# Performance work log

Measured on AMD Instinct MI355X. Metric: run time of the kernel, lower is better.

Reference implementation:

```python
import jax, jax.numpy as jnp
import numpy as np

NUM_HEADS = 4
NUM_GROUPS = 32
EPS = 1e-6


def group_norm(x, gamma, beta):
    # x: [b, c, h, w]
    b, c, h, w = x.shape
    xg = x.reshape(b, NUM_GROUPS, c // NUM_GROUPS, h, w)
    mu = xg.mean(axis=(2, 3, 4), keepdims=True)
    var = xg.var(axis=(2, 3, 4), keepdims=True)
    xn = ((xg - mu) * jax.lax.rsqrt(var + EPS)).reshape(b, c, h, w)
    return xn * gamma[None, :, None, None] + beta[None, :, None, None]


def conv1x1(x, W, b):
    # 1x1 conv == per-pixel channel matmul. W: [out_c, in_c], b: [out_c]
    return jnp.einsum('bchw,oc->bohw', x, W) + b[None, :, None, None]


def setup_inputs() -> dict:
    key = jax.random.key(0)
    ks = jax.random.split(key, 8)
    c = 256
    b, h, w = 1, 64, 64
    s = 1.0 / np.sqrt(c)
    return {
        'x_kv': jax.random.normal(ks[0], (b, c, h, w), dtype=jnp.float32),
        'gn_gamma': jnp.ones((c,), dtype=jnp.float32),
        'gn_beta': jnp.zeros((c,), dtype=jnp.float32),
        'Wq': jax.random.normal(ks[1], (c, c), dtype=jnp.float32) * s,
        'bq': jnp.zeros((c,), dtype=jnp.float32),
        'Wk': jax.random.normal(ks[2], (c, c), dtype=jnp.float32) * s,
        'bk': jnp.zeros((c,), dtype=jnp.float32),
        'Wv': jax.random.normal(ks[3], (c, c), dtype=jnp.float32) * s,
        'bv': jnp.zeros((c,), dtype=jnp.float32),
        'Wp': jax.random.normal(ks[4], (c, c), dtype=jnp.float32) * s,
        'bp': jnp.zeros((c,), dtype=jnp.float32),
    }


def reference(x_kv, gn_gamma, gn_beta, Wq, bq, Wk, bk, Wv, bv, Wp, bp):
    b, c, h, w = x_kv.shape
    hd = c // NUM_HEADS
    n = h * w

    h_norm = group_norm(x_kv, gn_gamma, gn_beta)  # self-attn: same norm for q,k,v

    q = conv1x1(h_norm, Wq, bq).reshape(b, NUM_HEADS, hd, n).transpose(0, 1, 3, 2)  # [b,H,n,hd]
    k = conv1x1(h_norm, Wk, bk).reshape(b, NUM_HEADS, hd, n)                        # [b,H,hd,n]
    v = conv1x1(h_norm, Wv, bv).reshape(b, NUM_HEADS, hd, n).transpose(0, 1, 3, 2)  # [b,H,n,hd]

    scores = jnp.einsum('bhnd,bhdm->bhnm', q, k) * (hd ** -0.5)  # [b,H,n,n]
    attn = jax.nn.softmax(scores, axis=-1)
    out = jnp.einsum('bhnm,bhmd->bhnd', attn, v)  # [b,H,n,hd]

    # Faithful to torch: permute(0,2,1,3).contiguous().view(b,c,h,w)
    out = out.transpose(0, 2, 1, 3).reshape(b, c, h, w)
    return x_kv + conv1x1(out, Wp, bp)
```

## Files before the change

### kernel.cpp

```cpp
#include <hip/hip_runtime.h>
#include <hip/hip_bf16.h>

#define NPIX 4096
#define CCH  256
#define HD   64
#define GSIZE 32768

typedef __bf16 bf16x8 __attribute__((ext_vector_type(8)));
typedef __bf16 bf16x4 __attribute__((ext_vector_type(4)));
typedef __bf16 bf16x2 __attribute__((ext_vector_type(2)));
typedef float  f32x4  __attribute__((ext_vector_type(4)));
typedef unsigned int uint32x4 __attribute__((ext_vector_type(4)));

#define XPITCH 264


__device__ __forceinline__ unsigned pack_bf16x2(float lo, float hi)
{
    bf16x2 v;
    v[0] = (__bf16)lo;
    v[1] = (__bf16)hi;
    return __builtin_bit_cast(unsigned, v);
}

__global__ __launch_bounds__(256) void stats_wconv(
    const float* __restrict__ X,
    const float* __restrict__ Wq, const float* __restrict__ Wk,
    const float* __restrict__ Wv, const float* __restrict__ Wp,
    float* __restrict__ psum, float* __restrict__ pssq, __bf16* __restrict__ Wb)
{
    const int bid = blockIdx.x, t = threadIdx.x;
    if (bid < 256) {
        const float* base = X + bid * 4096;
        float sum = 0.f, ssq = 0.f;
        #pragma unroll
        for (int k = 0; k < 4; ++k) {
            float4 v = *(const float4*)(base + t * 4 + k * 1024);
            sum += v.x + v.y + v.z + v.w;
            ssq += v.x * v.x + v.y * v.y + v.z * v.z + v.w * v.w;
        }
        #pragma unroll
        for (int off = 1; off < 64; off <<= 1) {
            sum += __shfl_xor(sum, off);
            ssq += __shfl_xor(ssq, off);
        }
        __shared__ float red[2][4];
        const int wv = t >> 6;
        if ((t & 63) == 0) { red[0][wv] = sum; red[1][wv] = ssq; }
        __syncthreads();
        if (t == 0) {
            psum[bid] = red[0][0] + red[0][1] + red[0][2] + red[0][3];
            pssq[bid] = red[1][0] + red[1][1] + red[1][2] + red[1][3];
        }
    } else {
        const int j0 = (bid - 256) * 4096 + t * 16;
        const int m  = j0 >> 16;
        const float* W = (m == 0) ? Wq : (m == 1) ? Wk : (m == 2) ? Wv : Wp;
        const float sc = (m == 0) ? 0.125f : 1.f;
        const int off = j0 & 65535;
        #pragma unroll
        for (int k = 0; k < 4; ++k) {
            float4 v = *(const float4*)(W + off + k * 4);
            bf16x4 o;
            o[0] = (__bf16)(v.x * sc); o[1] = (__bf16)(v.y * sc);
            o[2] = (__bf16)(v.z * sc); o[3] = (__bf16)(v.w * sc);
            *(bf16x4*)(Wb + m * 65536 + off + k * 4) = o;
        }
    }
}

__global__ __launch_bounds__(256) void gn_qkv(
    const float* __restrict__ X, const float* __restrict__ gamma,
    const float* __restrict__ beta,
    const float* __restrict__ psum, const float* __restrict__ pssq,
    const __bf16* __restrict__ Wb,
    const float* __restrict__ bq, const float* __restrict__ bk,
    const float* __restrict__ bv,
    __bf16* __restrict__ Qb, __bf16* __restrict__ Kb, __bf16* __restrict__ Vb)
{
    __shared__ __bf16 tile[64 * XPITCH];
    __shared__ float al[256], bl[256];

    const int t = threadIdx.x, lane = t & 63, wave = t >> 6;
    const int l16 = lane & 15, quad = lane >> 4;
    const int p0 = blockIdx.x * 64;
    const int z = blockIdx.y >> 1, och = blockIdx.y & 1;

    {
        const int g = t >> 3;
        float s = 0.f, q = 0.f;
        #pragma unroll
        for (int j = 0; j < 8; ++j) { s += psum[g * 8 + j]; q += pssq[g * 8 + j]; }
        const float mu  = s * (1.f / GSIZE);
        const float var = q * (1.f / GSIZE) - mu * mu;
        const float a = gamma[t] * rsqrtf(var + 1e-6f);
        al[t] = a;
        bl[t] = beta[t] - mu * a;
    }
    __syncthreads();

    #pragma unroll 4
    for (int i = 0; i < 16; ++i) {
        const int c4 = wave * 64 + i * 4;
        f32x4 a4 = *(const f32x4*)(al + c4);
        f32x4 b4 = *(const f32x4*)(bl + c4);
        bf16x4 pk;
        pk[0] = (__bf16)(X[(c4 + 0) * NPIX + p0 + lane] * a4[0] + b4[0]);
        pk[1] = (__bf16)(X[(c4 + 1) * NPIX + p0 + lane] * a4[1] + b4[1]);
        pk[2] = (__bf16)(X[(c4 + 2) * NPIX + p0 + lane] * a4[2] + b4[2]);
        pk[3] = (__bf16)(X[(c4 + 3) * NPIX + p0 + lane] * a4[3] + b4[3]);
        *(bf16x4*)(tile + lane * XPITCH + c4) = pk;
    }
    __syncthreads();

    const int pw = wave * 16;
    bf16x8 xf[8];
    #pragma unroll
    for (int kc = 0; kc < 8; ++kc)
        xf[kc] = *(const bf16x8*)(tile + (pw + l16) * XPITCH + kc * 32 + quad * 8);

    const __bf16* Wz = Wb + z * 65536;
    const float* bias = (z == 0) ? bq : (z == 1) ? bk : bv;

    if (z < 2) {
        const float qs = (z == 0) ? 0.125f : 1.f;
        __bf16* dst = (z == 0) ? Qb : Kb;
        #pragma unroll
        for (int grp = 0; grp < 2; ++grp) {
            f32x4 acc[4] = {};
            #pragma unroll
            for (int kc = 0; kc < 8; ++kc) {
                #pragma unroll
                for (int u = 0; u < 4; ++u) {
                    bf16x8 wf = *(const bf16x8*)(Wz + (och * 128 + (grp * 4 + u) * 16 + l16) * CCH + kc * 32 + quad * 8);
                    acc[u] = __builtin_amdgcn_mfma_f32_16x16x32_bf16(wf, xf[kc], acc[u], 0, 0, 0);
                }
            }
            #pragma unroll
            for (int u = 0; u < 4; ++u) {
                const int ot = och * 8 + grp * 4 + u;
                f32x4 bz = *(const f32x4*)(bias + och * 128 + (grp * 4 + u) * 16 + quad * 4);
                bf16x4 o;
                o[0] = (__bf16)(acc[u][0] + bz[0] * qs);
                o[1] = (__bf16)(acc[u][1] + bz[1] * qs);
                o[2] = (__bf16)(acc[u][2] + bz[2] * qs);
                o[3] = (__bf16)(acc[u][3] + bz[3] * qs);
                const int head = ot >> 2, dloc = (ot & 3) * 16 + quad * 4;
                *(bf16x4*)(dst + head * (NPIX * HD) + (p0 + pw + l16) * HD + dloc) = o;
            }
        }
    } else {
        #pragma unroll
        for (int grp = 0; grp < 2; ++grp) {
            f32x4 acc[4] = {};
            #pragma unroll
            for (int kc = 0; kc < 8; ++kc) {
                #pragma unroll
                for (int u = 0; u < 4; ++u) {
                    bf16x8 wf = *(const bf16x8*)(Wz + (och * 128 + (grp * 4 + u) * 16 + l16) * CCH + kc * 32 + quad * 8);
                    acc[u] = __builtin_amdgcn_mfma_f32_16x16x32_bf16(xf[kc], wf, acc[u], 0, 0, 0);
                }
            }
            #pragma unroll
            for (int u = 0; u < 4; ++u) {
                const int oc = och * 128 + (grp * 4 + u) * 16 + l16;
                const float bz = bias[oc];
                bf16x4 o;
                o[0] = (__bf16)(acc[u][0] + bz); o[1] = (__bf16)(acc[u][1] + bz);
                o[2] = (__bf16)(acc[u][2] + bz); o[3] = (__bf16)(acc[u][3] + bz);
                *(bf16x4*)(Vb + oc * NPIX + p0 + pw + quad * 4) = o;
            }
        }
    }
}

__global__ __launch_bounds__(256, 1) void attn_mfma(
    const __bf16* __restrict__ Qb, const __bf16* __restrict__ Kb,
    const __bf16* __restrict__ Vb, __bf16* __restrict__ Sb)
{
    __shared__ __align__(16) float co[4 * 64 * 68];
    __shared__ float cl[4 * 64];

    const int t = threadIdx.x, lane = t & 63, wave = t >> 6;
    const int l16 = lane & 15, quad = lane >> 4;

    const int bid  = blockIdx.x;
    const int head = (bid & 7) >> 1;
    const int qt   = ((bid >> 3) << 1) | (bid & 1);
    const int p0   = qt * 64;

    const __bf16* Qh = Qb + head * (NPIX * HD);
    const __bf16* Kh = Kb + head * (NPIX * HD) + (wave * 32 + l16) * HD + quad * 8;
    const __bf16* Vh = Vb + head * (HD * NPIX) + l16 * NPIX + wave * 32 + quad * 8;

    bf16x8 qf[4][2];
    #pragma unroll
    for (int rt = 0; rt < 4; ++rt) {
        const __bf16* qp = Qh + (p0 + rt * 16 + l16) * HD + quad * 8;
        qf[rt][0] = *(const bf16x8*)(qp);
        qf[rt][1] = *(const bf16x8*)(qp + 32);
    }

    bf16x8 ones;
    #pragma unroll
    for (int j = 0; j < 8; ++j) ones[j] = (__bf16)1.0f;

    f32x4 l_acc[4] = {};
    f32x4 o_acc[4][4] = {};

    auto ldKV = [&](int it, bf16x8 (&kf)[2][2], bf16x8 (&vf)[4]) {
        const __bf16* kp = Kh + it * (128 * HD);
        kf[0][0] = *(const bf16x8*)(kp);
        kf[0][1] = *(const bf16x8*)(kp + 32);
        kf[1][0] = *(const bf16x8*)(kp + 16 * HD);
        kf[1][1] = *(const bf16x8*)(kp + 16 * HD + 32);
        const __bf16* vp = Vh + it * 128;
        #pragma unroll
        for (int dt = 0; dt < 4; ++dt)
            vf[dt] = *(const bf16x8*)(vp + dt * (16 * NPIX));
    };

    auto step = [&](const bf16x8 (&kf)[2][2], const bf16x8 (&vf)[4]) {
        f32x4 st0[4] = {}, st1[4] = {};
        #pragma unroll
        for (int rt = 0; rt < 4; ++rt) {
            st0[rt] = __builtin_amdgcn_mfma_f32_16x16x32_bf16(kf[0][0], qf[rt][0], st0[rt], 0, 0, 0);
            st0[rt] = __builtin_amdgcn_mfma_f32_16x16x32_bf16(kf[0][1], qf[rt][1], st0[rt], 0, 0, 0);
            st1[rt] = __builtin_amdgcn_mfma_f32_16x16x32_bf16(kf[1][0], qf[rt][0], st1[rt], 0, 0, 0);
            st1[rt] = __builtin_amdgcn_mfma_f32_16x16x32_bf16(kf[1][1], qf[rt][1], st1[rt], 0, 0, 0);
        }
        #pragma unroll
        for (int rt = 0; rt < 4; ++rt) {
            unsigned a0 = pack_bf16x2(__expf(st0[rt][0]), __expf(st0[rt][1]));
            unsigned a1 = pack_bf16x2(__expf(st0[rt][2]), __expf(st0[rt][3]));
            unsigned b0 = pack_bf16x2(__expf(st1[rt][0]), __expf(st1[rt][1]));
            unsigned b1 = pack_bf16x2(__expf(st1[rt][2]), __expf(st1[rt][3]));
            asm("v_permlane32_swap_b32 %0, %1" : "+v"(a0), "+v"(b0));
            asm("v_permlane32_swap_b32 %0, %1" : "+v"(a1), "+v"(b1));
            asm("v_permlane16_swap_b32 %0, %1" : "+v"(a0), "+v"(b0));
            asm("v_permlane16_swap_b32 %0, %1" : "+v"(a1), "+v"(b1));
            uint32x4 w;
            w[0] = a0; w[1] = a1; w[2] = b0; w[3] = b1;
            const bf16x8 bp = __builtin_bit_cast(bf16x8, w);
            l_acc[rt] = __builtin_amdgcn_mfma_f32_16x16x32_bf16(ones, bp, l_acc[rt], 0, 0, 0);
            #pragma unroll
            for (int dt = 0; dt < 4; ++dt)
                o_acc[dt][rt] = __builtin_amdgcn_mfma_f32_16x16x32_bf16(vf[dt], bp, o_acc[dt][rt], 0, 0, 0);
        }
    };

    bf16x8 ka[2][2], va[4], kb[2][2], vb[4];
    ldKV(0, ka, va);
    #pragma unroll 1
    for (int it = 0; it < 32; it += 2) {
        ldKV(it + 1, kb, vb);
        step(ka, va);
        if (it + 2 < 32) ldKV(it + 2, ka, va);
        step(kb, vb);
    }

    #pragma unroll
    for (int dt = 0; dt < 4; ++dt)
        #pragma unroll
        for (int rt = 0; rt < 4; ++rt)
            *(f32x4*)(co + wave * 4352 + (rt * 16 + l16) * 68 + dt * 16 + quad * 4) = o_acc[dt][rt];
    if (quad == 0) {
        #pragma unroll
        for (int rt = 0; rt < 4; ++rt)
            cl[wave * 64 + rt * 16 + l16] = l_acc[rt][0];
    }
    __syncthreads();

    {
        const int row = t >> 2, dc = (t & 3) * 16;
        const float l = cl[row] + cl[64 + row] + cl[128 + row] + cl[192 + row];
        const float inv = 1.f / l;
        f32x4 s[4];
        #pragma unroll
        for (int j = 0; j < 4; ++j) {
            s[j] = f32x4{0.f, 0.f, 0.f, 0.f};
            #pragma unroll
            for (int w = 0; w < 4; ++w)
                s[j] += *(const f32x4*)(co + w * 4352 + row * 68 + dc + j * 4);
        }
        bf16x8 o1, o2;
        #pragma unroll
        for (int j = 0; j < 4; ++j) {
            o1[j]     = (__bf16)(s[0][j] * inv);
            o1[j + 4] = (__bf16)(s[1][j] * inv);
            o2[j]     = (__bf16)(s[2][j] * inv);
            o2[j + 4] = (__bf16)(s[3][j] * inv);
        }
        __bf16* dst = Sb + (p0 + row) * CCH + head * HD + dc;
        *(bf16x8*)(dst)     = o1;
        *(bf16x8*)(dst + 8) = o2;
    }
}

__global__ __launch_bounds__(256) void gemm_proj(
    const __bf16* __restrict__ Sb, const __bf16* __restrict__ Wpb,
    const float* __restrict__ bias, const float* __restrict__ X,
    float* __restrict__ Out)
{
    __shared__ __bf16 Bs[32 * XPITCH];

    const int t = threadIdx.x, lane = t & 63, wave = t >> 6;
    const int l16 = lane & 15, quad = lane >> 4;
    const int p0  = blockIdx.x * 32;
    const int och = blockIdx.y;

    #pragma unroll
    for (int pg = 0; pg < 4; ++pg) {
        bf16x8 v = *(const bf16x8*)(Sb + t * NPIX + p0 + pg * 8);
        #pragma unroll
        for (int j = 0; j < 8; ++j)
            Bs[(pg * 8 + j) * XPITCH + t] = v[j];
    }
    __syncthreads();

    const int pixset = wave & 1, ocset = wave >> 1;
    bf16x8 af[8];
    #pragma unroll
    for (int kc = 0; kc < 8; ++kc)
        af[kc] = *(const bf16x8*)(Bs + (pixset * 16 + l16) * XPITCH + kc * 32 + quad * 8);

    #pragma unroll
    for (int u = 0; u < 4; ++u) {
        f32x4 acc = {};
        const int oc_t = och * 128 + ocset * 64 + u * 16;
        #pragma unroll
        for (int kc = 0; kc < 8; ++kc) {
            bf16x8 wf = *(const bf16x8*)(Wpb + (oc_t + l16) * CCH + kc * 32 + quad * 8);
            acc = __builtin_amdgcn_mfma_f32_16x16x32_bf16(af[kc], wf, acc, 0, 0, 0);
        }
        const int oc  = oc_t + l16;
        const int pix = p0 + pixset * 16 + quad * 4;
        const float bz = bias[oc];
        f32x4 r4 = *(const f32x4*)(X + oc * NPIX + pix);
        f32x4 y;
        y[0] = acc[0] + bz + r4[0];
        y[1] = acc[1] + bz + r4[1];
        y[2] = acc[2] + bz + r4[2];
        y[3] = acc[3] + bz + r4[3];
        *(f32x4*)(Out + oc * NPIX + pix) = y;
    }
}

extern "C" void kernel_launch(void* const* d_in, const int* in_sizes, int n_in,
                              void* d_out, int out_size, void* d_ws, size_t ws_size,
                              hipStream_t stream)
{
    const float* x     = (const float*)d_in[0];
    const float* gamma = (const float*)d_in[1];
    const float* beta  = (const float*)d_in[2];
    const float* Wq    = (const float*)d_in[3];
    const float* bq    = (const float*)d_in[4];
    const float* Wk    = (const float*)d_in[5];
    const float* bk    = (const float*)d_in[6];
    const float* Wv    = (const float*)d_in[7];
    const float* bv    = (const float*)d_in[8];
    const float* Wp    = (const float*)d_in[9];
    const float* bp    = (const float*)d_in[10];
    float* out = (float*)d_out;

    char* ws = (char*)d_ws;
    float*  psum = (float*)(ws);
    float*  pssq = (float*)(ws + 1024);
    __bf16* Wb   = (__bf16*)(ws + 65536);
    __bf16* Qb   = (__bf16*)(ws + (1 << 20));
    __bf16* Kb   = (__bf16*)(ws + (3 << 20));
    __bf16* Vb   = (__bf16*)(ws + (5 << 20));
    __bf16* Sb   = (__bf16*)(ws + (7 << 20));

    stats_wconv<<<320, 256, 0, stream>>>(x, Wq, Wk, Wv, Wp, psum, pssq, Wb);

    dim3 gq(64, 6);
    gn_qkv<<<gq, 256, 0, stream>>>(x, gamma, beta, psum, pssq, Wb,
                                   bq, bk, bv, Qb, Kb, Vb);

    attn_mfma<<<256, 256, 0, stream>>>(Qb, Kb, Vb, Sb);

    dim3 gp(128, 2);
    gemm_proj<<<gp, 256, 0, stream>>>(Sb, Wb + 3 * 65536, bp, x, out);
}
```

Before: 140.5 us.

## Halve attention query tile to 32 rows, double grid, add MFMA priority hints

```diff
diff --git a/kernel.cpp b/kernel.cpp
--- a/kernel.cpp
+++ b/kernel.cpp
@@ -174,28 +174,28 @@
     }
 }
 
-__global__ __launch_bounds__(256, 1) void attn_mfma(
+__global__ __launch_bounds__(256, 2) void attn_mfma(
     const __bf16* __restrict__ Qb, const __bf16* __restrict__ Kb,
     const __bf16* __restrict__ Vb, __bf16* __restrict__ Sb)
 {
-    __shared__ __align__(16) float co[4 * 64 * 68];
-    __shared__ float cl[4 * 64];
+    __shared__ __align__(16) float co[4 * 32 * 68];
+    __shared__ float cl[4 * 32];
 
     const int t = threadIdx.x, lane = t & 63, wave = t >> 6;
     const int l16 = lane & 15, quad = lane >> 4;
 
     const int bid  = blockIdx.x;
     const int head = (bid & 7) >> 1;
-    const int qt   = ((bid >> 3) << 1) | (bid & 1);
-    const int p0   = qt * 64;
+    const int qidx = ((bid >> 3) << 1) | (bid & 1);
+    const int p0   = qidx * 32;
 
     const __bf16* Qh = Qb + head * (NPIX * HD);
     const __bf16* Kh = Kb + head * (NPIX * HD) + (wave * 32 + l16) * HD + quad * 8;
     const __bf16* Vh = Vb + head * (HD * NPIX) + l16 * NPIX + wave * 32 + quad * 8;
 
-    bf16x8 qf[4][2];
-    #pragma unroll
-    for (int rt = 0; rt < 4; ++rt) {
+    bf16x8 qf[2][2];
+    #pragma unroll
+    for (int rt = 0; rt < 2; ++rt) {
         const __bf16* qp = Qh + (p0 + rt * 16 + l16) * HD + quad * 8;
         qf[rt][0] = *(const bf16x8*)(qp);
         qf[rt][1] = *(const bf16x8*)(qp + 32);
@@ -205,8 +205,8 @@
     #pragma unroll
     for (int j = 0; j < 8; ++j) ones[j] = (__bf16)1.0f;
 
-    f32x4 l_acc[4] = {};
-    f32x4 o_acc[4][4] = {};
+    f32x4 l_acc[2] = {};
+    f32x4 o_acc[4][2] = {};
 
     auto ldKV = [&](int it, bf16x8 (&kf)[2][2], bf16x8 (&vf)[4]) {
         const __bf16* kp = Kh + it * (128 * HD);
@@ -221,16 +221,18 @@
     };
 
     auto step = [&](const bf16x8 (&kf)[2][2], const bf16x8 (&vf)[4]) {
-        f32x4 st0[4] = {}, st1[4] = {};
-        #pragma unroll
-        for (int rt = 0; rt < 4; ++rt) {
+        f32x4 st0[2] = {}, st1[2] = {};
+        __builtin_amdgcn_s_setprio(1);
+        #pragma unroll
+        for (int rt = 0; rt < 2; ++rt) {
             st0[rt] = __builtin_amdgcn_mfma_f32_16x16x32_bf16(kf[0][0], qf[rt][0], st0[rt], 0, 0, 0);
             st0[rt] = __builtin_amdgcn_mfma_f32_16x16x32_bf16(kf[0][1], qf[rt][1], st0[rt], 0, 0, 0);
             st1[rt] = __builtin_amdgcn_mfma_f32_16x16x32_bf16(kf[1][0], qf[rt][0], st1[rt], 0, 0, 0);
             st1[rt] = __builtin_amdgcn_mfma_f32_16x16x32_bf16(kf[1][1], qf[rt][1], st1[rt], 0, 0, 0);
         }
-        #pragma unroll
-        for (int rt = 0; rt < 4; ++rt) {
+        __builtin_amdgcn_s_setprio(0);
+        #pragma unroll
+        for (int rt = 0; rt < 2; ++rt) {
             unsigned a0 = pack_bf16x2(__expf(st0[rt][0]), __expf(st0[rt][1]));
             unsigned a1 = pack_bf16x2(__expf(st0[rt][2]), __expf(st0[rt][3]));
             unsigned b0 = pack_bf16x2(__expf(st1[rt][0]), __expf(st1[rt][1]));
@@ -242,10 +244,12 @@
             uint32x4 w;
             w[0] = a0; w[1] = a1; w[2] = b0; w[3] = b1;
             const bf16x8 bp = __builtin_bit_cast(bf16x8, w);
+            __builtin_amdgcn_s_setprio(1);
             l_acc[rt] = __builtin_amdgcn_mfma_f32_16x16x32_bf16(ones, bp, l_acc[rt], 0, 0, 0);
             #pragma unroll
             for (int dt = 0; dt < 4; ++dt)
                 o_acc[dt][rt] = __builtin_amdgcn_mfma_f32_16x16x32_bf16(vf[dt], bp, o_acc[dt][rt], 0, 0, 0);
+            __builtin_amdgcn_s_setprio(0);
         }
     };
 
@@ -262,38 +266,32 @@
     #pragma unroll
     for (int dt = 0; dt < 4; ++dt)
         #pragma unroll
-        for (int rt = 0; rt < 4; ++rt)
-            *(f32x4*)(co + wave * 4352 + (rt * 16 + l16) * 68 + dt * 16 + quad * 4) = o_acc[dt][rt];
+        for (int rt = 0; rt < 2; ++rt)
+            *(f32x4*)(co + wave * 2176 + (rt * 16 + l16) * 68 + dt * 16 + quad * 4) = o_acc[dt][rt];
     if (quad == 0) {
         #pragma unroll
-        for (int rt = 0; rt < 4; ++rt)
-            cl[wave * 64 + rt * 16 + l16] = l_acc[rt][0];
+        for (int rt = 0; rt < 2; ++rt)
+            cl[wave * 32 + rt * 16 + l16] = l_acc[rt][0];
     }
     __syncthreads();
 
     {
-        const int row = t >> 2, dc = (t & 3) * 16;
-        const float l = cl[row] + cl[64 + row] + cl[128 + row] + cl[192 + row];
+        const int row = t >> 3, dc = (t & 7) * 8;
+        const float l = cl[row] + cl[32 + row] + cl[64 + row] + cl[96 + row];
         const float inv = 1.f / l;
-        f32x4 s[4];
+        f32x4 s0 = {0.f, 0.f, 0.f, 0.f}, s1 = {0.f, 0.f, 0.f, 0.f};
+        #pragma unroll
+        for (int w = 0; w < 4; ++w) {
+            s0 += *(const f32x4*)(co + w * 2176 + row * 68 + dc);
+            s1 += *(const f32x4*)(co + w * 2176 + row * 68 + dc + 4);
+        }
+        bf16x8 o;
         #pragma unroll
         for (int j = 0; j < 4; ++j) {
-            s[j] = f32x4{0.f, 0.f, 0.f, 0.f};
-            #pragma unroll
-            for (int w = 0; w < 4; ++w)
-                s[j] += *(const f32x4*)(co + w * 4352 + row * 68 + dc + j * 4);
-        }
-        bf16x8 o1, o2;
-        #pragma unroll
-        for (int j = 0; j < 4; ++j) {
-            o1[j]     = (__bf16)(s[0][j] * inv);
-            o1[j + 4] = (__bf16)(s[1][j] * inv);
-            o2[j]     = (__bf16)(s[2][j] * inv);
-            o2[j + 4] = (__bf16)(s[3][j] * inv);
-        }
-        __bf16* dst = Sb + (p0 + row) * CCH + head * HD + dc;
-        *(bf16x8*)(dst)     = o1;
-        *(bf16x8*)(dst + 8) = o2;
+            o[j]     = (__bf16)(s0[j] * inv);
+            o[j + 4] = (__bf16)(s1[j] * inv);
+        }
+        *(bf16x8*)(Sb + (p0 + row) * CCH + head * HD + dc) = o;
     }
 }
 
@@ -378,7 +376,7 @@
     gn_qkv<<<gq, 256, 0, stream>>>(x, gamma, beta, psum, pssq, Wb,
                                    bq, bk, bv, Qb, Kb, Vb);
 
-    attn_mfma<<<256, 256, 0, stream>>>(Qb, Kb, Vb, Sb);
+    attn_mfma<<<512, 256, 0, stream>>>(Qb, Kb, Vb, Sb);
 
     dim3 gp(128, 2);
     gemm_proj<<<gp, 256, 0, stream>>>(Sb, Wb + 3 * 65536, bp, x, out);
```

New measurement: 167.5 us. 1.19x slower.

## Split attention over key halves with partial outputs and a merge kernel

Applied to the files above, without the earlier changes.

```diff
diff --git a/kernel.cpp b/kernel.cpp
--- a/kernel.cpp
+++ b/kernel.cpp
@@ -174,9 +174,10 @@
     }
 }
 
-__global__ __launch_bounds__(256, 1) void attn_mfma(
+__global__ __launch_bounds__(256, 2) void attn_partial(
     const __bf16* __restrict__ Qb, const __bf16* __restrict__ Kb,
-    const __bf16* __restrict__ Vb, __bf16* __restrict__ Sb)
+    const __bf16* __restrict__ Vb, float* __restrict__ Op,
+    float* __restrict__ Lp)
 {
     __shared__ __align__(16) float co[4 * 64 * 68];
     __shared__ float cl[4 * 64];
@@ -186,8 +187,10 @@
 
     const int bid  = blockIdx.x;
     const int head = (bid & 7) >> 1;
-    const int qt   = ((bid >> 3) << 1) | (bid & 1);
+    const int half = (bid >> 3) & 1;
+    const int qt   = ((bid >> 4) << 1) | (bid & 1);
     const int p0   = qt * 64;
+    const int kt0  = half * 16;
 
     const __bf16* Qh = Qb + head * (NPIX * HD);
     const __bf16* Kh = Kb + head * (NPIX * HD) + (wave * 32 + l16) * HD + quad * 8;
@@ -222,6 +225,7 @@
 
     auto step = [&](const bf16x8 (&kf)[2][2], const bf16x8 (&vf)[4]) {
         f32x4 st0[4] = {}, st1[4] = {};
+        __builtin_amdgcn_s_setprio(1);
         #pragma unroll
         for (int rt = 0; rt < 4; ++rt) {
             st0[rt] = __builtin_amdgcn_mfma_f32_16x16x32_bf16(kf[0][0], qf[rt][0], st0[rt], 0, 0, 0);
@@ -229,6 +233,7 @@
             st1[rt] = __builtin_amdgcn_mfma_f32_16x16x32_bf16(kf[1][0], qf[rt][0], st1[rt], 0, 0, 0);
             st1[rt] = __builtin_amdgcn_mfma_f32_16x16x32_bf16(kf[1][1], qf[rt][1], st1[rt], 0, 0, 0);
         }
+        __builtin_amdgcn_s_setprio(0);
         #pragma unroll
         for (int rt = 0; rt < 4; ++rt) {
             unsigned a0 = pack_bf16x2(__expf(st0[rt][0]), __expf(st0[rt][1]));
@@ -242,20 +247,24 @@
             uint32x4 w;
             w[0] = a0; w[1] = a1; w[2] = b0; w[3] = b1;
             const bf16x8 bp = __builtin_bit_cast(bf16x8, w);
+            __builtin_amdgcn_s_setprio(1);
             l_acc[rt] = __builtin_amdgcn_mfma_f32_16x16x32_bf16(ones, bp, l_acc[rt], 0, 0, 0);
             #pragma unroll
             for (int dt = 0; dt < 4; ++dt)
                 o_acc[dt][rt] = __builtin_amdgcn_mfma_f32_16x16x32_bf16(vf[dt], bp, o_acc[dt][rt], 0, 0, 0);
+            __builtin_amdgcn_s_setprio(0);
         }
     };
 
     bf16x8 ka[2][2], va[4], kb[2][2], vb[4];
-    ldKV(0, ka, va);
+    ldKV(kt0, ka, va);
     #pragma unroll 1
-    for (int it = 0; it < 32; it += 2) {
+    for (int it = kt0; it < kt0 + 16; it += 2) {
         ldKV(it + 1, kb, vb);
+        __builtin_amdgcn_sched_barrier(0);
         step(ka, va);
-        if (it + 2 < 32) ldKV(it + 2, ka, va);
+        if (it + 2 < kt0 + 16) ldKV(it + 2, ka, va);
+        __builtin_amdgcn_sched_barrier(0);
         step(kb, vb);
     }
 
@@ -273,8 +282,6 @@
 
     {
         const int row = t >> 2, dc = (t & 3) * 16;
-        const float l = cl[row] + cl[64 + row] + cl[128 + row] + cl[192 + row];
-        const float inv = 1.f / l;
         f32x4 s[4];
         #pragma unroll
         for (int j = 0; j < 4; ++j) {
@@ -283,18 +290,37 @@
             for (int w = 0; w < 4; ++w)
                 s[j] += *(const f32x4*)(co + w * 4352 + row * 68 + dc + j * 4);
         }
-        bf16x8 o1, o2;
-        #pragma unroll
-        for (int j = 0; j < 4; ++j) {
-            o1[j]     = (__bf16)(s[0][j] * inv);
-            o1[j + 4] = (__bf16)(s[1][j] * inv);
-            o2[j]     = (__bf16)(s[2][j] * inv);
-            o2[j + 4] = (__bf16)(s[3][j] * inv);
-        }
-        __bf16* dst = Sb + (p0 + row) * CCH + head * HD + dc;
-        *(bf16x8*)(dst)     = o1;
-        *(bf16x8*)(dst + 8) = o2;
-    }
+        float* dsto = Op + half * (NPIX * CCH) + (p0 + row) * CCH + head * HD + dc;
+        #pragma unroll
+        for (int j = 0; j < 4; ++j)
+            *(f32x4*)(dsto + j * 4) = s[j];
+        if ((t & 3) == 0) {
+            const float l = cl[row] + cl[64 + row] + cl[128 + row] + cl[192 + row];
+            Lp[half * 16384 + head * 4096 + p0 + row] = l;
+        }
+    }
+}
+
+__global__ __launch_bounds__(256) void attn_merge(
+    const float* __restrict__ Op, const float* __restrict__ Lp,
+    __bf16* __restrict__ Sb)
+{
+    const int idx = (blockIdx.x * 256 + threadIdx.x) * 8;
+    const int P = idx >> 8;
+    const int head = (idx >> 6) & 3;
+    const float l = Lp[head * 4096 + P] + Lp[16384 + head * 4096 + P];
+    const float inv = 1.f / l;
+    f32x4 a0 = *(const f32x4*)(Op + idx);
+    f32x4 a1 = *(const f32x4*)(Op + idx + 4);
+    f32x4 b0 = *(const f32x4*)(Op + NPIX * CCH + idx);
+    f32x4 b1 = *(const f32x4*)(Op + NPIX * CCH + idx + 4);
+    bf16x8 o;
+    #pragma unroll
+    for (int j = 0; j < 4; ++j) {
+        o[j]     = (__bf16)((a0[j] + b0[j]) * inv);
+        o[j + 4] = (__bf16)((a1[j] + b1[j]) * inv);
+    }
+    *(bf16x8*)(Sb + idx) = o;
 }
 
 __global__ __launch_bounds__(256) void gemm_proj(
@@ -371,6 +397,8 @@
     __bf16* Kb   = (__bf16*)(ws + (3 << 20));
     __bf16* Vb   = (__bf16*)(ws + (5 << 20));
     __bf16* Sb   = (__bf16*)(ws + (7 << 20));
+    float*  Op   = (float*)(ws + (16 << 20));
+    float*  Lp   = (float*)(ws + (25 << 20));
 
     stats_wconv<<<320, 256, 0, stream>>>(x, Wq, Wk, Wv, Wp, psum, pssq, Wb);
 
@@ -378,7 +406,8 @@
     gn_qkv<<<gq, 256, 0, stream>>>(x, gamma, beta, psum, pssq, Wb,
                                    bq, bk, bv, Qb, Kb, Vb);
 
-    attn_mfma<<<256, 256, 0, stream>>>(Qb, Kb, Vb, Sb);
+    attn_partial<<<512, 256, 0, stream>>>(Qb, Kb, Vb, Op, Lp);
+    attn_merge<<<512, 256, 0, stream>>>(Op, Lp, Sb);
 
     dim3 gp(128, 2);
     gemm_proj<<<gp, 256, 0, stream>>>(Sb, Wb + 3 * 65536, bp, x, out);
```

After: 147.0 us. 4.7% more time.

## Triple-buffer K/V register prefetch and fold log2e into Q scale for exp2

Applied to the files above, without the earlier changes.

```diff
diff --git a/kernel.cpp b/kernel.cpp
--- a/kernel.cpp
+++ b/kernel.cpp
@@ -5,6 +5,8 @@
 #define CCH  256
 #define HD   64
 #define GSIZE 32768
+
+#define QSCALE 0.18033688f
 
 typedef __bf16 bf16x8 __attribute__((ext_vector_type(8)));
 typedef __bf16 bf16x4 __attribute__((ext_vector_type(4)));
@@ -13,6 +15,12 @@
 typedef unsigned int uint32x4 __attribute__((ext_vector_type(4)));
 
 #define XPITCH 264
+
+#if __has_builtin(__builtin_amdgcn_exp2f)
+#define EXP2(x) __builtin_amdgcn_exp2f(x)
+#else
+#define EXP2(x) __expf((x) * 0.6931471805599453f)
+#endif
 
 
 __device__ __forceinline__ unsigned pack_bf16x2(float lo, float hi)
@@ -56,7 +64,7 @@
         const int j0 = (bid - 256) * 4096 + t * 16;
         const int m  = j0 >> 16;
         const float* W = (m == 0) ? Wq : (m == 1) ? Wk : (m == 2) ? Wv : Wp;
-        const float sc = (m == 0) ? 0.125f : 1.f;
+        const float sc = (m == 0) ? QSCALE : 1.f;
         const int off = j0 & 65535;
         #pragma unroll
         for (int k = 0; k < 4; ++k) {
@@ -123,7 +131,7 @@
     const float* bias = (z == 0) ? bq : (z == 1) ? bk : bv;
 
     if (z < 2) {
-        const float qs = (z == 0) ? 0.125f : 1.f;
+        const float qs = (z == 0) ? QSCALE : 1.f;
         __bf16* dst = (z == 0) ? Qb : Kb;
         #pragma unroll
         for (int grp = 0; grp < 2; ++grp) {
@@ -208,33 +216,37 @@
     f32x4 l_acc[4] = {};
     f32x4 o_acc[4][4] = {};
 
-    auto ldKV = [&](int it, bf16x8 (&kf)[2][2], bf16x8 (&vf)[4]) {
+    auto ldKV = [&](int it,
+                    bf16x8& k0, bf16x8& k1, bf16x8& k2, bf16x8& k3,
+                    bf16x8& v0, bf16x8& v1, bf16x8& v2, bf16x8& v3) {
         const __bf16* kp = Kh + it * (128 * HD);
-        kf[0][0] = *(const bf16x8*)(kp);
-        kf[0][1] = *(const bf16x8*)(kp + 32);
-        kf[1][0] = *(const bf16x8*)(kp + 16 * HD);
-        kf[1][1] = *(const bf16x8*)(kp + 16 * HD + 32);
+        k0 = *(const bf16x8*)(kp);
+        k1 = *(const bf16x8*)(kp + 32);
+        k2 = *(const bf16x8*)(kp + 16 * HD);
+        k3 = *(const bf16x8*)(kp + 16 * HD + 32);
         const __bf16* vp = Vh + it * 128;
-        #pragma unroll
-        for (int dt = 0; dt < 4; ++dt)
-            vf[dt] = *(const bf16x8*)(vp + dt * (16 * NPIX));
+        v0 = *(const bf16x8*)(vp);
+        v1 = *(const bf16x8*)(vp + 16 * NPIX);
+        v2 = *(const bf16x8*)(vp + 32 * NPIX);
+        v3 = *(const bf16x8*)(vp + 48 * NPIX);
     };
 
-    auto step = [&](const bf16x8 (&kf)[2][2], const bf16x8 (&vf)[4]) {
+    auto step = [&](bf16x8 k0, bf16x8 k1, bf16x8 k2, bf16x8 k3,
+                    bf16x8 v0, bf16x8 v1, bf16x8 v2, bf16x8 v3) {
         f32x4 st0[4] = {}, st1[4] = {};
         #pragma unroll
         for (int rt = 0; rt < 4; ++rt) {
-            st0[rt] = __builtin_amdgcn_mfma_f32_16x16x32_bf16(kf[0][0], qf[rt][0], st0[rt], 0, 0, 0);
-            st0[rt] = __builtin_amdgcn_mfma_f32_16x16x32_bf16(kf[0][1], qf[rt][1], st0[rt], 0, 0, 0);
-            st1[rt] = __builtin_amdgcn_mfma_f32_16x16x32_bf16(kf[1][0], qf[rt][0], st1[rt], 0, 0, 0);
-            st1[rt] = __builtin_amdgcn_mfma_f32_16x16x32_bf16(kf[1][1], qf[rt][1], st1[rt], 0, 0, 0);
+            st0[rt] = __builtin_amdgcn_mfma_f32_16x16x32_bf16(k0, qf[rt][0], st0[rt], 0, 0, 0);
+            st0[rt] = __builtin_amdgcn_mfma_f32_16x16x32_bf16(k1, qf[rt][1], st0[rt], 0, 0, 0);
+            st1[rt] = __builtin_amdgcn_mfma_f32_16x16x32_bf16(k2, qf[rt][0], st1[rt], 0, 0, 0);
+            st1[rt] = __builtin_amdgcn_mfma_f32_16x16x32_bf16(k3, qf[rt][1], st1[rt], 0, 0, 0);
         }
         #pragma unroll
         for (int rt = 0; rt < 4; ++rt) {
-            unsigned a0 = pack_bf16x2(__expf(st0[rt][0]), __expf(st0[rt][1]));
-            unsigned a1 = pack_bf16x2(__expf(st0[rt][2]), __expf(st0[rt][3]));
-            unsigned b0 = pack_bf16x2(__expf(st1[rt][0]), __expf(st1[rt][1]));
-            unsigned b1 = pack_bf16x2(__expf(st1[rt][2]), __expf(st1[rt][3]));
+            unsigned a0 = pack_bf16x2(EXP2(st0[rt][0]), EXP2(st0[rt][1]));
+            unsigned a1 = pack_bf16x2(EXP2(st0[rt][2]), EXP2(st0[rt][3]));
+            unsigned b0 = pack_bf16x2(EXP2(st1[rt][0]), EXP2(st1[rt][1]));
+            unsigned b1 = pack_bf16x2(EXP2(st1[rt][2]), EXP2(st1[rt][3]));
             asm("v_permlane32_swap_b32 %0, %1" : "+v"(a0), "+v"(b0));
             asm("v_permlane32_swap_b32 %0, %1" : "+v"(a1), "+v"(b1));
             asm("v_permlane16_swap_b32 %0, %1" : "+v"(a0), "+v"(b0));
@@ -243,21 +255,31 @@
             w[0] = a0; w[1] = a1; w[2] = b0; w[3] = b1;
             const bf16x8 bp = __builtin_bit_cast(bf16x8, w);
             l_acc[rt] = __builtin_amdgcn_mfma_f32_16x16x32_bf16(ones, bp, l_acc[rt], 0, 0, 0);
-            #pragma unroll
-            for (int dt = 0; dt < 4; ++dt)
-                o_acc[dt][rt] = __builtin_amdgcn_mfma_f32_16x16x32_bf16(vf[dt], bp, o_acc[dt][rt], 0, 0, 0);
+            o_acc[0][rt] = __builtin_amdgcn_mfma_f32_16x16x32_bf16(v0, bp, o_acc[0][rt], 0, 0, 0);
+            o_acc[1][rt] = __builtin_amdgcn_mfma_f32_16x16x32_bf16(v1, bp, o_acc[1][rt], 0, 0, 0);
+            o_acc[2][rt] = __builtin_amdgcn_mfma_f32_16x16x32_bf16(v2, bp, o_acc[2][rt], 0, 0, 0);
+            o_acc[3][rt] = __builtin_amdgcn_mfma_f32_16x16x32_bf16(v3, bp, o_acc[3][rt], 0, 0, 0);
         }
     };
 
-    bf16x8 ka[2][2], va[4], kb[2][2], vb[4];
-    ldKV(0, ka, va);
+    bf16x8 ka0, ka1, ka2, ka3, va0, va1, va2, va3;
+    bf16x8 kb0, kb1, kb2, kb3, vb0, vb1, vb2, vb3;
+    bf16x8 kc0, kc1, kc2, kc3, vc0, vc1, vc2, vc3;
+
+    ldKV(0, ka0, ka1, ka2, ka3, va0, va1, va2, va3);
+    ldKV(1, kb0, kb1, kb2, kb3, vb0, vb1, vb2, vb3);
+
     #pragma unroll 1
-    for (int it = 0; it < 32; it += 2) {
-        ldKV(it + 1, kb, vb);
-        step(ka, va);
-        if (it + 2 < 32) ldKV(it + 2, ka, va);
-        step(kb, vb);
-    }
+    for (int it = 0; it < 30; it += 3) {
+        ldKV(it + 2, kc0, kc1, kc2, kc3, vc0, vc1, vc2, vc3);
+        step(ka0, ka1, ka2, ka3, va0, va1, va2, va3);
+        ldKV(it + 3, ka0, ka1, ka2, ka3, va0, va1, va2, va3);
+        step(kb0, kb1, kb2, kb3, vb0, vb1, vb2, vb3);
+        ldKV(it + 4, kb0, kb1, kb2, kb3, vb0, vb1, vb2, vb3);
+        step(kc0, kc1, kc2, kc3, vc0, vc1, vc2, vc3);
+    }
+    step(ka0, ka1, ka2, ka3, va0, va1, va2, va3);
+    step(kb0, kb1, kb2, kb3, vb0, vb1, vb2, vb3);
 
     #pragma unroll
     for (int dt = 0; dt < 4; ++dt)
```

New measurement: 140.9 us. Within noise of the previous version (+0.3%).
